# Optimization experiments

Measured on AMD Instinct MI355X. Metric: run time of the kernel, lower is better.

Reference implementation:

```python
import jax, jax.numpy as jnp
from jax import lax
import numpy as np

N, M, S = 16, 32, 128
ALPHA = 1e-06


def _conv(x, w, b, stride):
    y = lax.conv_general_dilated(x, w, (stride, stride), [(1, 1), (1, 1)],
                                 dimension_numbers=('NCHW', 'OIHW', 'NCHW'))
    return y + b[None, :, None, None]


def _deconv(x, w, b):
    # torch ConvTranspose2d(k=4, s=2, p=1); torch weight layout [in, out, kh, kw]
    k = jnp.transpose(w, (1, 0, 2, 3))[:, :, ::-1, ::-1]
    y = lax.conv_general_dilated(x, k, (1, 1), [(2, 2), (2, 2)],
                                 lhs_dilation=(2, 2),
                                 dimension_numbers=('NCHW', 'OIHW', 'NCHW'))
    return y + b[None, :, None, None]


def _kaiming(key, shape):
    fan_in = shape[1] * shape[2] * shape[3]
    return jax.random.normal(key, shape, dtype=jnp.float32) * np.float32(np.sqrt(2.0 / fan_in))


def setup_inputs():
    key = jax.random.key(0)
    ks = jax.random.split(key, 12)
    B, H, W = 8, 256, 256
    return {
        'x': jax.random.normal(ks[0], (B, 3, H, W), dtype=jnp.float32),
        'e0n_w1': _kaiming(ks[1], (N, 3, 3, 3)), 'e0n_b1': jnp.zeros((N,), jnp.float32),
        'e0n_w2': _kaiming(ks[2], (N, N, 3, 3)), 'e0n_b2': jnp.zeros((N,), jnp.float32),
        'e0s_w1': _kaiming(ks[3], (S, 3, 3, 3)), 'e0s_b1': jnp.zeros((S,), jnp.float32),
        'e0s_w2': _kaiming(ks[4], (S, S, 3, 3)), 'e0s_b2': jnp.zeros((S,), jnp.float32),
        'd0_dw': jax.random.normal(ks[5], (S, 3, 4, 4), jnp.float32) * np.float32(np.sqrt(2.0 / (3 * 16))),
        'd0_db': jnp.zeros((3,), jnp.float32),
        'd0_cw': _kaiming(ks[6], (3, 3, 3, 3)), 'd0_cb': jnp.zeros((3,), jnp.float32),
        'cell_k': jax.random.normal(ks[7], (M, N), jnp.float32) / np.float32(np.sqrt(N)),
        'cell_v': jax.random.normal(ks[8], (M, S), jnp.float32) / np.float32(np.sqrt(S)),
    }


def reference(x, e0n_w1, e0n_b1, e0n_w2, e0n_b2, e0s_w1, e0s_b1, e0s_w2, e0s_b2,
              d0_dw, d0_db, d0_cw, d0_cb, cell_k, cell_v):
    silu = jax.nn.silu
    # ConvBlock encoders (stride-2 on second conv)
    e0_n = silu(_conv(silu(_conv(x, e0n_w1, e0n_b1, 1)), e0n_w2, e0n_b2, 2))  # [B,N,H/2,W/2]
    e0_s = silu(_conv(silu(_conv(x, e0s_w1, e0s_b1, 1)), e0s_w2, e0s_b2, 2))  # [B,S,H/2,W/2]
    B, _, H, W = e0_n.shape
    # permute+flatten to token streams (the irregular-access glue)
    z = e0_n.transpose(0, 2, 3, 1).reshape(-1, N)        # [T, N]
    t_star = e0_s.transpose(0, 2, 3, 1).reshape(-1, S)   # [T, S]
    # memcell: softmax key/value retrieval over M slots
    w = jax.nn.softmax(z @ cell_k.T / jnp.sqrt(jnp.float32(N)), axis=-1)  # [T, M]
    t_hat = w @ cell_v                                   # read_update's read (old memory)
    cell_v_new = cell_v + ALPHA * (w.T @ (t_star - t_hat))  # delta-rule value update
    t_read = w @ cell_v_new                              # read(); d1_n == e0_n so weights reused
    d0_m = t_read.reshape(B, H, W, S).transpose(0, 3, 1, 2)  # [B,S,H/2,W/2]
    # DeconvBlock decoder back to 3 channels at full resolution
    d0_n = silu(_conv(silu(_deconv(d0_m, d0_dw, d0_db)), d0_cw, d0_cb, 1))
    return d0_n
```

## Files before the change

kernel.cpp:

```cpp
#include <hip/hip_runtime.h>
#include <hip/hip_bf16.h>


#define ALPHA_F 1e-6f
#define TTOT 131072

typedef __attribute__((ext_vector_type(8))) short bf16x8;
typedef __attribute__((ext_vector_type(4))) float f32x4;

__device__ __forceinline__ float silu_f(float x) {
    return x * __builtin_amdgcn_rcpf(1.f + __expf(-x));
}

__device__ __forceinline__ short f2bf(float f) {
    __hip_bfloat16 h = __float2bfloat16(f);
    union { __hip_bfloat16 b; short s; } u; u.b = h; return u.s;
}

__device__ __forceinline__ float bf2f(unsigned short s) {
    union { unsigned u; float f; } c; c.u = (unsigned)s << 16; return c.f;
}

__device__ __forceinline__ int pack_fp8x4(float a, float b, float c, float d) {
    int lo = __builtin_amdgcn_cvt_pk_fp8_f32(a, b, 0, false);
    return  __builtin_amdgcn_cvt_pk_fp8_f32(c, d, lo, true);
}

template<int CO>
__global__ __launch_bounds__(256) void conv1_silu(
    const float* __restrict__ x, const float* __restrict__ wgt,
    const float* __restrict__ bias, float* __restrict__ out)
{
    int idx = blockIdx.x * 256 + threadIdx.x;
    int w = idx & 255, h = (idx >> 8) & 255, b = idx >> 16;
    const float* xb = x + (size_t)b * 3 * 65536;
    float in[27];
#pragma unroll
    for (int ci = 0; ci < 3; ci++)
#pragma unroll
        for (int ky = 0; ky < 3; ky++)
#pragma unroll
            for (int kx = 0; kx < 3; kx++) {
                int hh = h + ky - 1, ww = w + kx - 1;
                bool ok = ((unsigned)hh < 256u) && ((unsigned)ww < 256u);
                in[(ci * 3 + ky) * 3 + kx] = ok ? xb[(ci << 16) + (hh << 8) + ww] : 0.f;
            }
    float* ob = out + (size_t)b * CO * 65536 + (h << 8) + w;
#pragma unroll 4
    for (int co = 0; co < CO; co++) {
        float acc = bias[co];
#pragma unroll
        for (int k = 0; k < 27; k++) acc += in[k] * wgt[co * 27 + k];
        ob[(size_t)co << 16] = silu_f(acc);
    }
}

#define C1K 40
__global__ __launch_bounds__(256) void conv1s_mfma(
    const float* __restrict__ x, const float* __restrict__ wgt,
    const float* __restrict__ bias, char* __restrict__ out8)
{
    __shared__ __align__(16) short Ps[128 * C1K];
    __shared__ __align__(16) short Ws[64 * C1K];
    int tid = threadIdx.x;
    int g = blockIdx.x;
    int b = g >> 10, rem = g & 1023;
    int hh2 = rem >> 1;
    int h = hh2 >> 1, w0 = (hh2 & 1) * 128;
    int coB = (rem & 1) * 64;

    union { short s[32]; float4 v4[4]; } row;
#pragma unroll
    for (int k = 0; k < 32; k++) row.s[k] = 0;
    if (tid < 128) {
        int wpix = w0 + tid;
        const float* xb = x + (size_t)b * 3 * 65536;
#pragma unroll
        for (int ci = 0; ci < 3; ci++)
#pragma unroll
            for (int ky = 0; ky < 3; ky++)
#pragma unroll
                for (int kx = 0; kx < 3; kx++) {
                    int hhp = h + ky - 1, ww = wpix + kx - 1;
                    float v = 0.f;
                    if (((unsigned)hhp < 256u) && ((unsigned)ww < 256u))
                        v = xb[(ci << 16) + (hhp << 8) + ww];
                    row.s[ci * 9 + ky * 3 + kx] = f2bf(v);
                }
#pragma unroll
        for (int j = 0; j < 4; j++) *(float4*)&Ps[tid * C1K + j * 8] = row.v4[j];
    } else if (tid < 192) {
        int co = tid - 128;
#pragma unroll
        for (int k = 0; k < 27; k++) row.s[k] = f2bf(wgt[(coB + co) * 27 + k]);
#pragma unroll
        for (int j = 0; j < 4; j++) *(float4*)&Ws[co * C1K + j * 8] = row.v4[j];
    }
    __syncthreads();

    int lane = tid & 63, wave = tid >> 6;
    int coL = (wave & 1) * 32, pxH = (wave >> 1) * 64;
    int r16 = lane & 15, q = lane >> 4, koff = q * 8;
    bf16x8 af[2], bfr[4];
#pragma unroll
    for (int mt = 0; mt < 2; mt++)
        af[mt] = *(bf16x8*)&Ws[(coL + mt * 16 + r16) * C1K + koff];
#pragma unroll
    for (int nt = 0; nt < 4; nt++)
        bfr[nt] = *(bf16x8*)&Ps[(pxH + nt * 16 + r16) * C1K + koff];
    f32x4 acc[2][4];
#pragma unroll
    for (int mt = 0; mt < 2; mt++)
#pragma unroll
        for (int nt = 0; nt < 4; nt++) {
#pragma unroll
            for (int r = 0; r < 4; r++) acc[mt][nt][r] = 0.f;
            acc[mt][nt] = __builtin_amdgcn_mfma_f32_16x16x32_bf16(
                af[mt], bfr[nt], acc[mt][nt], 0, 0, 0);
        }

    int hwb = (h << 8) + w0 + pxH;
    int* ob4 = (int*)out8 + (size_t)b * 8 * 65536 * 4;
#pragma unroll
    for (int mt = 0; mt < 2; mt++) {
        int cb = coB + coL + mt * 16 + q * 4;
        float4 bv = *(const float4*)&bias[cb];
        int cg = (coB + coL + mt * 16) >> 4;
#pragma unroll
        for (int nt = 0; nt < 4; nt++) {
            int hw = hwb + nt * 16 + r16;
            int pk = pack_fp8x4(silu_f(acc[mt][nt][0] + bv.x),
                                silu_f(acc[mt][nt][1] + bv.y),
                                silu_f(acc[mt][nt][2] + bv.z),
                                silu_f(acc[mt][nt][3] + bv.w));
            ob4[((size_t)cg * 65536 + hw) * 4 + q] = pk;
        }
    }
}

__global__ __launch_bounds__(256) void wprep_kern(
    const float* __restrict__ w, int* __restrict__ wt8)
{
    int d = blockIdx.x * 256 + threadIdx.x;
    int pos = d >> 12;
    int rb = (d << 2) & 16383;
    int c16 = rb >> 11, co = (rb >> 4) & 127, e0 = rb & 15;
    float f[4];
#pragma unroll
    for (int j = 0; j < 4; j++) {
        int ci = c16 * 16 + e0 + j;
        f[j] = w[co * 1152 + ci * 9 + pos];
    }
    wt8[d] = pack_fp8x4(f[0], f[1], f[2], f[3]);
}

__global__ __launch_bounds__(256) void conv2s_mfma(
    const char* __restrict__ a8,
    const char* __restrict__ wt8,
    const float* __restrict__ bias, __hip_bfloat16* __restrict__ out)
{
    __shared__ __align__(16) char As[4 * 64 * 16];
    __shared__ __align__(16) char Bs[4 * 128 * 16];
    int tid = threadIdx.x;
    int g = blockIdx.x;
    int b = g >> 8, h2 = (g >> 1) & 127, w2base = (g & 1) * 64;
    int lane = tid & 63, wave = tid >> 6;
    int mrow = lane & 15, q = lane >> 4;

    f32x4 acc[2][4];
#pragma unroll
    for (int i = 0; i < 2; i++)
#pragma unroll
        for (int j = 0; j < 4; j++)
#pragma unroll
            for (int r = 0; r < 4; r++) acc[i][j][r] = 0.f;

    const float4* ab4 = (const float4*)a8 + (size_t)b * 8 * 65536;
    const float4* wb4 = (const float4*)wt8;
    int cA = tid >> 6, tokA = tid & 63;
    int sB0 = tid, sB1 = tid + 256;

#pragma unroll 1
    for (int pos = 0; pos < 9; pos++) {
        int ky = pos / 3, kx = pos - 3 * ky;
        int y = 2 * h2 - 1 + ky;
        if ((unsigned)y >= 256u) continue;
        int x = 2 * (w2base + tokA) - 1 + kx;
        int pix = (y << 8) + (x & 255);
#pragma unroll 1
        for (int cc = 0; cc < 2; cc++) {
            float4 a0 = make_float4(0.f, 0.f, 0.f, 0.f);
            if (x >= 0) a0 = ab4[(size_t)(cc * 4 + cA) * 65536 + pix];
            const float4* brow = wb4 + pos * 1024 + cc * 512;
            float4 b0 = brow[sB0], b1 = brow[sB1];
            __syncthreads();
            *(float4*)&As[tid * 16] = a0;
            *(float4*)&Bs[sB0 * 16] = b0;
            *(float4*)&Bs[sB1 * 16] = b1;
            __syncthreads();
#pragma unroll
            for (int kc = 0; kc < 2; kc++) {
                int cl = kc * 2 + (q >> 1), off = (q & 1) * 8;
                long afr[4], bfr[2];
#pragma unroll
                for (int mt = 0; mt < 4; mt++)
                    afr[mt] = *(long*)&As[(cl * 64 + mt * 16 + mrow) * 16 + off];
#pragma unroll
                for (int nt = 0; nt < 2; nt++)
                    bfr[nt] = *(long*)&Bs[(cl * 128 + wave * 32 + nt * 16 + mrow) * 16 + off];
#pragma unroll
                for (int nt = 0; nt < 2; nt++)
#pragma unroll
                    for (int mt = 0; mt < 4; mt++)
                        acc[nt][mt] = __builtin_amdgcn_mfma_f32_16x16x32_fp8_fp8(
                            afr[mt], bfr[nt], acc[nt][mt], 0, 0, 0);
            }
        }
    }
    int rowg = q * 4;
    size_t tbase = (size_t)g * 64;
#pragma unroll
    for (int nt = 0; nt < 2; nt++) {
        int co = wave * 32 + nt * 16 + mrow;
        float bvs = bias[co];
#pragma unroll
        for (int mt = 0; mt < 4; mt++)
#pragma unroll
            for (int r = 0; r < 4; r++) {
                int m = mt * 16 + rowg + r;
                out[(tbase + m) * 128 + co] =
                    __float2bfloat16(silu_f(acc[nt][mt][r] + bvs));
            }
    }
}

__global__ __launch_bounds__(256) void conv2n_fused(
    const float* __restrict__ in, const float* __restrict__ wgt,
    const float* __restrict__ bias, const float* __restrict__ ck,
    float* __restrict__ wout)
{
    int idx = blockIdx.x * 256 + threadIdx.x;
    int w2 = idx & 127, h2 = (idx >> 7) & 127, b = idx >> 14;
    const float* ib = in + (size_t)b * 16 * 65536;
    float acc[16];
#pragma unroll
    for (int co = 0; co < 16; co++) acc[co] = bias[co];
    int h0 = 2 * h2 - 1, w0 = 2 * w2 - 1;
    for (int ci = 0; ci < 16; ci++) {
        float t[9];
#pragma unroll
        for (int ky = 0; ky < 3; ky++)
#pragma unroll
            for (int kx = 0; kx < 3; kx++) {
                int hh = h0 + ky, ww = w0 + kx;
                bool ok = ((unsigned)hh < 256u) && ((unsigned)ww < 256u);
                t[ky * 3 + kx] = ok ? ib[((size_t)ci << 16) + (hh << 8) + ww] : 0.f;
            }
#pragma unroll
        for (int co = 0; co < 16; co++)
#pragma unroll
            for (int k = 0; k < 9; k++)
                acc[co] += t[k] * wgt[(co * 16 + ci) * 9 + k];
    }
    float zv[16];
#pragma unroll
    for (int co = 0; co < 16; co++) zv[co] = silu_f(acc[co]);
    float lg[32]; float mx = -1e30f;
#pragma unroll
    for (int m = 0; m < 32; m++) {
        float a = 0.f;
#pragma unroll
        for (int n = 0; n < 16; n++) a += zv[n] * ck[m * 16 + n];
        a *= 0.25f;
        lg[m] = a; mx = fmaxf(mx, a);
    }
    float s = 0.f;
#pragma unroll
    for (int m = 0; m < 32; m++) { lg[m] = __expf(lg[m] - mx); s += lg[m]; }
    float inv = 1.f / s;
    float4* wp = (float4*)(wout + (size_t)idx * 32);
#pragma unroll
    for (int m = 0; m < 8; m++)
        wp[m] = make_float4(lg[4 * m] * inv, lg[4 * m + 1] * inv,
                            lg[4 * m + 2] * inv, lg[4 * m + 3] * inv);
}

__global__ __launch_bounds__(256) void memcell_acc_kern(
    const float* __restrict__ wmat, const __hip_bfloat16* __restrict__ tstar,
    float* __restrict__ part)
{
    __shared__ float ws[64][32];
    __shared__ float ts[64 * 128];
    int tid = threadIdx.x;
    int sg = tid & 31, mg = tid >> 5;
    int mW = tid & 31, m2 = (tid >> 5) * 4;
    float accT[16], accW[4];
#pragma unroll
    for (int i = 0; i < 16; i++) accT[i] = 0.f;
#pragma unroll
    for (int i = 0; i < 4; i++) accW[i] = 0.f;

#pragma unroll 1
    for (int cc = 0; cc < 2; cc++) {
        int c = blockIdx.x * 2 + cc;
        size_t base = (size_t)c * 64;
        __syncthreads();
        {
            const float4* src = (const float4*)(wmat + base * 32);
            float4* dst = (float4*)&ws[0][0];
#pragma unroll
            for (int i = 0; i < 2; i++) dst[tid + 256 * i] = src[tid + 256 * i];
            const float4* src2 = (const float4*)(tstar + base * 128);
#pragma unroll
            for (int i = 0; i < 4; i++) {
                union { float4 v; unsigned short us[8]; } u;
                u.v = src2[tid + 256 * i];
                float* d = &ts[(tid + 256 * i) * 8];
                float4 lo = make_float4(bf2f(u.us[0]), bf2f(u.us[1]), bf2f(u.us[2]), bf2f(u.us[3]));
                float4 hi = make_float4(bf2f(u.us[4]), bf2f(u.us[5]), bf2f(u.us[6]), bf2f(u.us[7]));
                *(float4*)d = lo; *(float4*)(d + 4) = hi;
            }
        }
        __syncthreads();
        for (int t = 0; t < 64; t++) {
            float4 wv = *(const float4*)&ws[t][mg * 4];
            float4 sv = *(const float4*)&ts[t * 128 + sg * 4];
            accT[0]  += wv.x * sv.x; accT[1]  += wv.x * sv.y; accT[2]  += wv.x * sv.z; accT[3]  += wv.x * sv.w;
            accT[4]  += wv.y * sv.x; accT[5]  += wv.y * sv.y; accT[6]  += wv.y * sv.z; accT[7]  += wv.y * sv.w;
            accT[8]  += wv.z * sv.x; accT[9]  += wv.z * sv.y; accT[10] += wv.z * sv.z; accT[11] += wv.z * sv.w;
            accT[12] += wv.w * sv.x; accT[13] += wv.w * sv.y; accT[14] += wv.w * sv.z; accT[15] += wv.w * sv.w;
            float wa = ws[t][mW];
            float4 wb = *(const float4*)&ws[t][m2];
            accW[0] += wa * wb.x; accW[1] += wa * wb.y;
            accW[2] += wa * wb.z; accW[3] += wa * wb.w;
        }
    }
    float* pb = part + (size_t)blockIdx.x * 5120;
#pragma unroll
    for (int i = 0; i < 16; i++) pb[i * 256 + tid] = accT[i];
#pragma unroll
    for (int i = 0; i < 4; i++) pb[4096 + i * 256 + tid] = accW[i];
}

__global__ __launch_bounds__(256) void memcell_reduce_kern(
    const float* __restrict__ part, float* __restrict__ WtT, float* __restrict__ WtW)
{
    int gid = blockIdx.x * 256 + threadIdx.x;
    int j = gid % 5120, seg = gid / 5120;
    const float* p = part + (size_t)seg * 64 * 5120 + j;
    float s = 0.f;
#pragma unroll 8
    for (int k = 0; k < 64; k++) s += p[(size_t)k * 5120];
    int i = j >> 8, t = j & 255;
    if (j < 4096) {
        int sg = t & 31, mg = t >> 5;
        atomicAdd(&WtT[(mg * 4 + (i >> 2)) * 128 + sg * 4 + (i & 3)], s);
    } else {
        int i2 = i - 16;
        int mW = t & 31, m2 = (t >> 5) * 4;
        atomicAdd(&WtW[mW * 32 + m2 + i2], s);
    }
}

__global__ __launch_bounds__(256) void cvnew_kern(
    const float* __restrict__ cv, const float* __restrict__ WtW,
    const float* __restrict__ WtT, float* __restrict__ cvn)
{
    int idx = blockIdx.x * 256 + threadIdx.x;
    int s = idx & 127, m = idx >> 7;
    float g = WtT[idx];
#pragma unroll
    for (int j = 0; j < 32; j++) g -= WtW[m * 32 + j] * cv[j * 128 + s];
    cvn[idx] = cv[idx] + ALPHA_F * g;
}

__global__ __launch_bounds__(256) void emat_kern(
    const float* __restrict__ cvn, const float* __restrict__ dw, float* __restrict__ E)
{
    int idx = blockIdx.x * 256 + threadIdx.x;
    int m = idx >> 6, j = idx & 63;
    int pos = j >> 2, co = j & 3;
    float s = 0.f;
    if (co < 3) {
        const float* cv = cvn + m * 128;
        for (int ci = 0; ci < 128; ci++)
            s += cv[ci] * dw[ci * 48 + co * 16 + pos];
    }
    E[idx] = s;
}

__global__ __launch_bounds__(256) void tread64_kern(
    const float* __restrict__ wmat, const float* __restrict__ E, float* __restrict__ t64)
{
    int t = blockIdx.x * 256 + threadIdx.x;
    float wv[32];
    const float4* wp = (const float4*)(wmat + (size_t)t * 32);
#pragma unroll
    for (int i = 0; i < 8; i++) {
        float4 v = wp[i];
        wv[4 * i] = v.x; wv[4 * i + 1] = v.y; wv[4 * i + 2] = v.z; wv[4 * i + 3] = v.w;
    }
    f32x4 acc[16];
#pragma unroll
    for (int i = 0; i < 16; i++)
#pragma unroll
        for (int r = 0; r < 4; r++) acc[i][r] = 0.f;
    const f32x4* E4 = (const f32x4*)E;
#pragma unroll 4
    for (int m = 0; m < 32; m++) {
        float wm = wv[m];
#pragma unroll
        for (int i = 0; i < 16; i++) {
            f32x4 e = E4[m * 16 + i];
#pragma unroll
            for (int r = 0; r < 4; r++) acc[i][r] += wm * e[r];
        }
    }
    f32x4* ob = (f32x4*)t64;
#pragma unroll
    for (int i = 0; i < 16; i++)
        ob[(size_t)i * TTOT + t] = acc[i];
}

__global__ __launch_bounds__(256) void dec_gather_kern(
    const float* __restrict__ t64, const float* __restrict__ db, float* __restrict__ out)
{
    int g = blockIdx.x;
    int wb = g & 7, hb = (g >> 3) & 7, b = g >> 6;
    int tx = threadIdx.x & 15, ty = threadIdx.x >> 4;
    int h2 = hb * 16 + ty, w2 = wb * 16 + tx;

    float mh[3], mw[3];
    int ihc[3], iwc[3];
#pragma unroll
    for (int a = 0; a < 3; a++) {
        int v = h2 - 1 + a;
        mh[a] = ((unsigned)v < 128u) ? 1.f : 0.f;
        ihc[a] = v < 0 ? 0 : (v > 127 ? 127 : v);
        v = w2 - 1 + a;
        mw[a] = ((unsigned)v < 128u) ? 1.f : 0.f;
        iwc[a] = v < 0 ? 0 : (v > 127 ? 127 : v);
    }
    float acc[2][2][3];
#pragma unroll
    for (int ph = 0; ph < 2; ph++)
#pragma unroll
        for (int pw = 0; pw < 2; pw++)
#pragma unroll
            for (int co = 0; co < 3; co++) acc[ph][pw][co] = db[co];

    const int RA[4] = {0, 1, 1, 2}, RP[4] = {0, 0, 1, 1}, RK[4] = {3, 1, 2, 0};
    size_t tokb = (size_t)b * 16384;
#pragma unroll
    for (int ri = 0; ri < 4; ri++)
#pragma unroll
        for (int cj = 0; cj < 4; cj++) {
            int a = RA[ri], c = RA[cj];
            float m = mh[a] * mw[c];
            size_t tok = tokb + (ihc[a] << 7) + iwc[c];
            int pos = RK[ri] * 4 + RK[cj];
            float4 v = *(const float4*)&t64[((size_t)pos * TTOT + tok) * 4];
            int ph = RP[ri], pw = RP[cj];
            acc[ph][pw][0] += m * v.x;
            acc[ph][pw][1] += m * v.y;
            acc[ph][pw][2] += m * v.z;
        }
    int h = 2 * h2, w = 2 * w2;
#pragma unroll
    for (int ph = 0; ph < 2; ph++)
#pragma unroll
        for (int co = 0; co < 3; co++) {
            float2 v = make_float2(silu_f(acc[ph][0][co]), silu_f(acc[ph][1][co]));
            *(float2*)&out[(size_t)b * 3 * 65536 + (size_t)co * 65536 + ((size_t)(h + ph) << 8) + w] = v;
        }
}

extern "C" void kernel_launch(void* const* d_in, const int* in_sizes, int n_in,
                              void* d_out, int out_size, void* d_ws, size_t ws_size,
                              hipStream_t stream)
{
    const float* x      = (const float*)d_in[0];
    const float* e0n_w1 = (const float*)d_in[1];
    const float* e0n_b1 = (const float*)d_in[2];
    const float* e0n_w2 = (const float*)d_in[3];
    const float* e0n_b2 = (const float*)d_in[4];
    const float* e0s_w1 = (const float*)d_in[5];
    const float* e0s_b1 = (const float*)d_in[6];
    const float* e0s_w2 = (const float*)d_in[7];
    const float* e0s_b2 = (const float*)d_in[8];
    const float* d0_dw  = (const float*)d_in[9];
    const float* d0_db  = (const float*)d_in[10];
    const float* d0_cw  = (const float*)d_in[11];
    const float* d0_cb  = (const float*)d_in[12];
    const float* cell_k = (const float*)d_in[13];
    const float* cell_v = (const float*)d_in[14];
    float* outp = (float*)d_out;

    char* ws = (char*)d_ws;
    char* a_s8             = ws;
    __hip_bfloat16* t_star = (__hip_bfloat16*)(ws + 134217728);
    float* a_n    = (float*)(ws + 201326592);
    char* wt8     = (char*)(ws + 201326592);
    float* part   = (float*)(ws + 201850880);
    float* Emat   = (float*)(ws + 224000000);
    float* wmat   = (float*)(ws + 243269632);
    float* WtW    = (float*)(ws + 260046848);
    float* WtT    = (float*)(ws + 260050944);
    float* cvn    = (float*)(ws + 260067328);
    float* t64    = (float*)(ws);
    float* dec1   = (float*)(ws + 67108864);

    conv1_silu<16><<<2048, 256, 0, stream>>>(x, e0n_w1, e0n_b1, a_n);
    conv2n_fused<<<512, 256, 0, stream>>>(a_n, e0n_w2, e0n_b2, cell_k, wmat);
    wprep_kern<<<144, 256, 0, stream>>>(e0s_w2, (int*)wt8);
    conv1s_mfma<<<8192, 256, 0, stream>>>(x, e0s_w1, e0s_b1, a_s8);
    conv2s_mfma<<<2048, 256, 0, stream>>>(a_s8, wt8, e0s_b2, t_star);
    hipMemsetAsync(WtW, 0, (1024 + 4096) * sizeof(float), stream);
    memcell_acc_kern<<<1024, 256, 0, stream>>>(wmat, t_star, part);
    memcell_reduce_kern<<<320, 256, 0, stream>>>(part, WtT, WtW);
    cvnew_kern<<<16, 256, 0, stream>>>(cell_v, WtW, WtT, cvn);
    emat_kern<<<8, 256, 0, stream>>>(cvn, d0_dw, Emat);
    tread64_kern<<<512, 256, 0, stream>>>(wmat, Emat, t64);
    dec_gather_kern<<<512, 256, 0, stream>>>(t64, d0_db, dec1);
    conv1_silu<3><<<2048, 256, 0, stream>>>(dec1, d0_cw, d0_cb, outp);
}
```

Before: 296.7 us.

## Store first-layer N activations in bf16 and merge conv2s channel chunks per position

A dedicated first-layer kernel for the N-branch now writes its SiLU activations as bf16 instead of fp32. The stride-2 fused conv that follows reads them as bf16, which halves the bytes written and read for that intermediate; the buffer moves to a non-overlapping workspace slot. The fp8 MFMA conv2s kernel now stages both 64-channel chunks for a kernel position at once in a doubled LDS buffer. That halves the barrier pairs and loop iterations, at the cost of more shared memory per block. Rounding the activations to bf16 adds a small precision loss before the second conv.

```diff
diff --git a/kernel.cpp b/kernel.cpp
--- a/kernel.cpp
+++ b/kernel.cpp
@@ -55,6 +55,34 @@
     }
 }
 
+__global__ __launch_bounds__(256) void conv1n_kern(
+    const float* __restrict__ x, const float* __restrict__ wgt,
+    const float* __restrict__ bias, __hip_bfloat16* __restrict__ out)
+{
+    int idx = blockIdx.x * 256 + threadIdx.x;
+    int w = idx & 255, h = (idx >> 8) & 255, b = idx >> 16;
+    const float* xb = x + (size_t)b * 3 * 65536;
+    float in[27];
+#pragma unroll
+    for (int ci = 0; ci < 3; ci++)
+#pragma unroll
+        for (int ky = 0; ky < 3; ky++)
+#pragma unroll
+            for (int kx = 0; kx < 3; kx++) {
+                int hh = h + ky - 1, ww = w + kx - 1;
+                bool ok = ((unsigned)hh < 256u) && ((unsigned)ww < 256u);
+                in[(ci * 3 + ky) * 3 + kx] = ok ? xb[(ci << 16) + (hh << 8) + ww] : 0.f;
+            }
+    __hip_bfloat16* ob = out + (size_t)b * 16 * 65536 + (h << 8) + w;
+#pragma unroll 4
+    for (int co = 0; co < 16; co++) {
+        float acc = bias[co];
+#pragma unroll
+        for (int k = 0; k < 27; k++) acc += in[k] * wgt[co * 27 + k];
+        ob[(size_t)co << 16] = __float2bfloat16(silu_f(acc));
+    }
+}
+
 #define C1K 40
 __global__ __launch_bounds__(256) void conv1s_mfma(
     const float* __restrict__ x, const float* __restrict__ wgt,
@@ -159,8 +187,8 @@
     const char* __restrict__ wt8,
     const float* __restrict__ bias, __hip_bfloat16* __restrict__ out)
 {
-    __shared__ __align__(16) char As[4 * 64 * 16];
-    __shared__ __align__(16) char Bs[4 * 128 * 16];
+    __shared__ __align__(16) char As[8 * 64 * 16];
+    __shared__ __align__(16) char Bs[8 * 128 * 16];
     int tid = threadIdx.x;
     int g = blockIdx.x;
     int b = g >> 8, h2 = (g >> 1) & 127, w2base = (g & 1) * 64;
@@ -177,8 +205,8 @@
 
     const float4* ab4 = (const float4*)a8 + (size_t)b * 8 * 65536;
     const float4* wb4 = (const float4*)wt8;
-    int cA = tid >> 6, tokA = tid & 63;
-    int sB0 = tid, sB1 = tid + 256;
+    int cA0 = tid >> 6, tokA = tid & 63;
+    int sB0 = tid, sB1 = tid + 256, sB2 = tid + 512, sB3 = tid + 768;
 
 #pragma unroll 1
     for (int pos = 0; pos < 9; pos++) {
@@ -187,34 +215,38 @@
         if ((unsigned)y >= 256u) continue;
         int x = 2 * (w2base + tokA) - 1 + kx;
         int pix = (y << 8) + (x & 255);
-#pragma unroll 1
-        for (int cc = 0; cc < 2; cc++) {
-            float4 a0 = make_float4(0.f, 0.f, 0.f, 0.f);
-            if (x >= 0) a0 = ab4[(size_t)(cc * 4 + cA) * 65536 + pix];
-            const float4* brow = wb4 + pos * 1024 + cc * 512;
-            float4 b0 = brow[sB0], b1 = brow[sB1];
-            __syncthreads();
-            *(float4*)&As[tid * 16] = a0;
-            *(float4*)&Bs[sB0 * 16] = b0;
-            *(float4*)&Bs[sB1 * 16] = b1;
-            __syncthreads();
-#pragma unroll
-            for (int kc = 0; kc < 2; kc++) {
-                int cl = kc * 2 + (q >> 1), off = (q & 1) * 8;
-                long afr[4], bfr[2];
+        const float4* brow = wb4 + pos * 1024;
+        float4 a0 = make_float4(0.f, 0.f, 0.f, 0.f), a1 = a0;
+        if (x >= 0) {
+            a0 = ab4[(size_t)cA0 * 65536 + pix];
+            a1 = ab4[(size_t)(cA0 + 4) * 65536 + pix];
+        }
+        float4 b0 = brow[sB0], b1 = brow[sB1];
+        __syncthreads();
+        *(float4*)&As[tid * 16]         = a0;
+        *(float4*)&As[(tid + 256) * 16] = a1;
+        *(float4*)&Bs[sB0 * 16] = b0;
+        *(float4*)&Bs[sB1 * 16] = b1;
+        float4 b2 = brow[sB2], b3 = brow[sB3];
+        *(float4*)&Bs[sB2 * 16] = b2;
+        *(float4*)&Bs[sB3 * 16] = b3;
+        __syncthreads();
+#pragma unroll
+        for (int kc = 0; kc < 4; kc++) {
+            int cl = kc * 2 + (q >> 1), off = (q & 1) * 8;
+            long afr[4], bfr[2];
+#pragma unroll
+            for (int mt = 0; mt < 4; mt++)
+                afr[mt] = *(long*)&As[(cl * 64 + mt * 16 + mrow) * 16 + off];
+#pragma unroll
+            for (int nt = 0; nt < 2; nt++)
+                bfr[nt] = *(long*)&Bs[(cl * 128 + wave * 32 + nt * 16 + mrow) * 16 + off];
+#pragma unroll
+            for (int nt = 0; nt < 2; nt++)
 #pragma unroll
                 for (int mt = 0; mt < 4; mt++)
-                    afr[mt] = *(long*)&As[(cl * 64 + mt * 16 + mrow) * 16 + off];
-#pragma unroll
-                for (int nt = 0; nt < 2; nt++)
-                    bfr[nt] = *(long*)&Bs[(cl * 128 + wave * 32 + nt * 16 + mrow) * 16 + off];
-#pragma unroll
-                for (int nt = 0; nt < 2; nt++)
-#pragma unroll
-                    for (int mt = 0; mt < 4; mt++)
-                        acc[nt][mt] = __builtin_amdgcn_mfma_f32_16x16x32_fp8_fp8(
-                            afr[mt], bfr[nt], acc[nt][mt], 0, 0, 0);
-            }
+                    acc[nt][mt] = __builtin_amdgcn_mfma_f32_16x16x32_fp8_fp8(
+                        afr[mt], bfr[nt], acc[nt][mt], 0, 0, 0);
         }
     }
     int rowg = q * 4;
@@ -235,13 +267,13 @@
 }
 
 __global__ __launch_bounds__(256) void conv2n_fused(
-    const float* __restrict__ in, const float* __restrict__ wgt,
+    const __hip_bfloat16* __restrict__ in, const float* __restrict__ wgt,
     const float* __restrict__ bias, const float* __restrict__ ck,
     float* __restrict__ wout)
 {
     int idx = blockIdx.x * 256 + threadIdx.x;
     int w2 = idx & 127, h2 = (idx >> 7) & 127, b = idx >> 14;
-    const float* ib = in + (size_t)b * 16 * 65536;
+    const __hip_bfloat16* ib = in + (size_t)b * 16 * 65536;
     float acc[16];
 #pragma unroll
     for (int co = 0; co < 16; co++) acc[co] = bias[co];
@@ -254,7 +286,7 @@
             for (int kx = 0; kx < 3; kx++) {
                 int hh = h0 + ky, ww = w0 + kx;
                 bool ok = ((unsigned)hh < 256u) && ((unsigned)ww < 256u);
-                t[ky * 3 + kx] = ok ? ib[((size_t)ci << 16) + (hh << 8) + ww] : 0.f;
+                t[ky * 3 + kx] = ok ? __bfloat162float(ib[((size_t)ci << 16) + (hh << 8) + ww]) : 0.f;
             }
 #pragma unroll
         for (int co = 0; co < 16; co++)
@@ -499,7 +531,7 @@
     char* ws = (char*)d_ws;
     char* a_s8             = ws;
     __hip_bfloat16* t_star = (__hip_bfloat16*)(ws + 134217728);
-    float* a_n    = (float*)(ws + 201326592);
+    __hip_bfloat16* a_n    = (__hip_bfloat16*)(ws + 167772160);
     char* wt8     = (char*)(ws + 201326592);
     float* part   = (float*)(ws + 201850880);
     float* Emat   = (float*)(ws + 224000000);
@@ -510,7 +542,7 @@
     float* t64    = (float*)(ws);
     float* dec1   = (float*)(ws + 67108864);
 
-    conv1_silu<16><<<2048, 256, 0, stream>>>(x, e0n_w1, e0n_b1, a_n);
+    conv1n_kern<<<2048, 256, 0, stream>>>(x, e0n_w1, e0n_b1, a_n);
     conv2n_fused<<<512, 256, 0, stream>>>(a_n, e0n_w2, e0n_b2, cell_k, wmat);
     wprep_kern<<<144, 256, 0, stream>>>(e0s_w2, (int*)wt8);
     conv1s_mfma<<<8192, 256, 0, stream>>>(x, e0s_w1, e0s_b1, a_s8);
```

Measured after the change: 300.5 us. Within noise of the previous version (+1.3%).
